# Kernel tuning notes

Measured on AMD Instinct MI355X. Metric: run time of the kernel, lower is better.

Reference implementation:

```python
import jax, jax.numpy as jnp
import numpy as np

THRESHOLD = 1.25
CURRENT_DECAY = 0.25
VOLTAGE_DECAY = 0.03
SPIKE_PROB = 0.2


def setup_inputs() -> dict:
    key = jax.random.key(0)
    k1, k2 = jax.random.split(key)
    B, N, T = 2048, 16, 1024
    # binary input spike trains [batch, neurons, time]
    spike = (jax.random.uniform(k1, (B, N, T)) < SPIKE_PROB).astype(jnp.float32)
    # Dense synapse weight [out, in], no bias (lava-dl Dense default)
    W = jax.random.normal(k2, (N, N), dtype=jnp.float32) / np.sqrt(N)
    return {"spike": spike, "W": W}


def _cuba_dense(spike, W):
    # synaptic current input per timestep: z[b,o,t]
    z = jnp.einsum('oi,bit->bot', W, spike)
    zt = jnp.moveaxis(z, -1, 0)  # [T, B, O] for scan over time

    def step(carry, x):
        c, v = carry
        c = c * (1.0 - CURRENT_DECAY) + x
        v = v * (1.0 - VOLTAGE_DECAY) + c
        s = (v >= THRESHOLD).astype(v.dtype)
        v = v * (1.0 - s)  # hard reset to zero on spike
        return (c, v), s

    zero = jnp.zeros_like(zt[0])
    _, s = jax.lax.scan(step, (zero, zero), zt)  # s: [T, B, O]
    return jnp.moveaxis(s, 0, -1)  # [B, O, T]


def reference(spike, W):
    y = _cuba_dense(spike, W)  # [B, O, T] binary spikes
    # log-cosh free energy: exp(sum_neurons log(2 cosh(y))) -> [B, T]
    return jnp.exp(jnp.sum(jnp.log(2.0 * jnp.cosh(y)), axis=1))
```

## Files before the change

kernel.cpp:

```cpp
#include <hip/hip_runtime.h>
#include <stdint.h>

#define T_STEPS 1024
#define NWORDS  256
#define NB      8
#define SCAN_BLOCK (NB * 16)

typedef float f32x4 __attribute__((ext_vector_type(4)));

__global__ __launch_bounds__(256) void k_maskify(const float* __restrict__ spike,
                                                 unsigned long long* __restrict__ masks,
                                                 const float* __restrict__ W,
                                                 double* __restrict__ tab,
                                                 int B) {
    const int b  = blockIdx.x;
    const int tc = threadIdx.x;
    if (b < B) {
        const float4* sp = reinterpret_cast<const float4*>(spike) + (size_t)b * (16 * NWORDS);
        unsigned int m0 = 0, m1 = 0, m2 = 0, m3 = 0;
#pragma unroll
        for (int i = 0; i < 16; ++i) {
            float4 v = sp[i * NWORDS + tc];
            m0 |= (v.x >= 0.5f) ? (1u << i) : 0u;
            m1 |= (v.y >= 0.5f) ? (1u << i) : 0u;
            m2 |= (v.z >= 0.5f) ? (1u << i) : 0u;
            m3 |= (v.w >= 0.5f) ? (1u << i) : 0u;
        }
        masks[(size_t)b * NWORDS + tc] =
            (unsigned long long)m0 | ((unsigned long long)m1 << 16) |
            ((unsigned long long)m2 << 32) | ((unsigned long long)m3 << 48);
    } else {
        const int o = tc & 15;
        double w[16];
#pragma unroll
        for (int j = 0; j < 16; ++j) w[j] = (double)W[o * 16 + j];
#pragma unroll
        for (int k = 0; k < 32; ++k) {
            const int e    = tc + k * 256;
            const int byte = (e >> 4) & 255;
            const int s    = k >> 4;
            double slo = 0.0, shi = 0.0;
#pragma unroll
            for (int j = 0; j < 4; ++j) slo += (byte & (1 << j))  ? w[8 * s + j]     : 0.0;
#pragma unroll
            for (int j = 0; j < 4; ++j) shi += (byte & (16 << j)) ? w[8 * s + 4 + j] : 0.0;
            tab[s * 4096 + byte * 16 + o] = slo + shi;
        }
    }
}

__global__ __launch_bounds__(SCAN_BLOCK, 1) void k_scan(const double* __restrict__ tab,
                                                        const unsigned long long* __restrict__ masks,
                                                        float* __restrict__ out) {
    const int tid = threadIdx.x;
    const int bb  = tid >> 4;
    const int o   = tid & 15;
    const int b   = blockIdx.x * NB + bb;

    const uint64_t tb     = (uint64_t)tab;
    const uint64_t mb     = (uint64_t)masks;
    const uint64_t ob_out = (uint64_t)out;
    const uint32_t ob0    = (uint32_t)(o * 8);
    const uint32_t ob1    = ob0 + 32768u;
    const uint32_t vb_m   = (uint32_t)(b * (NWORDS * 8));
    const uint32_t vb_out = (uint32_t)(b * (T_STEPS * 4));
    const int grp_sh      = tid & 48;
    const bool writer     = (o == 0);

    double c = 0.0, v = 0.0;

    double TA_0, TA_1, TA_2, TA_3, TA_4, TA_5, TA_6, TA_7;
    double TB_0, TB_1, TB_2, TB_3, TB_4, TB_5, TB_6, TB_7;
    unsigned long long MA, MB, MC, MD, q0, q1;

#define GLT(DST, VOFF) \
    asm volatile("global_load_dwordx2 %0, %1, %2" : "=v"(DST) : "v"(VOFF), "s"(tb))
#define GLM(DST, IDX) do { int _mi = (IDX); if (_mi > 255) _mi = 255;                 \
    const uint32_t _vo = vb_m + ((uint32_t)_mi << 3);                                 \
    asm volatile("global_load_dwordx2 %0, %1, %2" : "=v"(DST) : "v"(_vo), "s"(mb)); } while (0)
#define WAITV(N) asm volatile("s_waitcnt vmcnt(" #N ")" ::: "memory")
#define SBAR __builtin_amdgcn_sched_barrier(0)

#define TISSUE(P, MW) do {                                                            \
    const uint32_t _lo = (uint32_t)(MW), _hi = (uint32_t)((MW) >> 32);                \
    uint32_t _a;                                                                      \
    _a = ob0 + ((_lo & 255u) << 7);          GLT(P##_0, _a);                          \
    _a = ob1 + (((_lo >> 8) & 255u) << 7);   GLT(P##_1, _a);                          \
    _a = ob0 + (((_lo >> 16) & 255u) << 7);  GLT(P##_2, _a);                          \
    _a = ob1 + ((_lo >> 24) << 7);           GLT(P##_3, _a);                          \
    _a = ob0 + ((_hi & 255u) << 7);          GLT(P##_4, _a);                          \
    _a = ob1 + (((_hi >> 8) & 255u) << 7);   GLT(P##_5, _a);                          \
    _a = ob0 + (((_hi >> 16) & 255u) << 7);  GLT(P##_6, _a);                          \
    _a = ob1 + ((_hi >> 24) << 7);           GLT(P##_7, _a);                          \
} while (0)

#define ZSTEP(ZL, ZH, OWEL) do {                                                      \
    const double _z = (ZL) + (ZH);                                                    \
    c = fma(c, 0.75, _z);                                                             \
    v = fma(v, 0.97, c);                                                              \
    const bool _s = (v >= 1.25);                                                      \
    const unsigned long long _bal = __ballot(_s);                                     \
    v = _s ? 0.0 : v;                                                                 \
    const uint32_t _k = __popc((uint32_t)(_bal >> grp_sh) & 0xFFFFu);                 \
    OWEL = exp2f(fmaf((float)_k, 0.62581400f, 16.0f));                                \
} while (0)

#define COMPUTE(P, WD) do {                                                           \
    f32x4 _ow;                                                                        \
    ZSTEP(P##_0, P##_1, _ow.x);                                                       \
    ZSTEP(P##_2, P##_3, _ow.y);                                                       \
    ZSTEP(P##_4, P##_5, _ow.z);                                                       \
    ZSTEP(P##_6, P##_7, _ow.w);                                                       \
    if (writer) {                                                                     \
        const uint32_t _vo = vb_out + ((uint32_t)(WD) << 4);                          \
        asm volatile("global_store_dwordx4 %0, %1, %2"                                \
                     :: "v"(_vo), "v"(_ow), "s"(ob_out) : "memory");                  \
    }                                                                                 \
} while (0)

#define BODY(WD, P, MU, MI) do {                                                      \
    GLM(MI, (WD) + 4);                                                                \
    WAITV(11); SBAR;                                                                  \
    COMPUTE(P, WD);                                                                   \
    TISSUE(P, MU); SBAR;                                                              \
} while (0)

    asm volatile("s_waitcnt vmcnt(0) lgkmcnt(0)" ::: "memory");

    GLM(q0, 0); GLM(q1, 1); GLM(MA, 2); GLM(MB, 3);
    WAITV(2); SBAR;
    TISSUE(TA, q0);
    TISSUE(TB, q1); SBAR;

    GLM(MC, 4);
    WAITV(9); SBAR;
    COMPUTE(TA, 0);
    TISSUE(TA, MA); SBAR;

    GLM(MD, 5);
    WAITV(11); SBAR;
    COMPUTE(TB, 1);
    TISSUE(TB, MB); SBAR;

    for (int w = 2; w < 254; w += 4) {
        BODY(w,     TA, MC, MA);
        BODY(w + 1, TB, MD, MB);
        BODY(w + 2, TA, MA, MC);
        BODY(w + 3, TB, MB, MD);
    }

    WAITV(10); SBAR;
    COMPUTE(TA, 254);
    WAITV(1); SBAR;
    COMPUTE(TB, 255);
    asm volatile("s_waitcnt vmcnt(0)" ::: "memory");

#undef GLT
#undef GLM
#undef WAITV
#undef SBAR
#undef TISSUE
#undef ZSTEP
#undef COMPUTE
#undef BODY
}

__global__ __launch_bounds__(SCAN_BLOCK) void k_scan_fb(const float* __restrict__ W,
                                                        const float* __restrict__ spike,
                                                        float* __restrict__ out) {
    __shared__ double ztab[4][16][16];
    __shared__ unsigned long long mlds[NB][NWORDS];
    __shared__ float outtab[17];
    const int tid = threadIdx.x, bb = tid >> 4, o = tid & 15;
    for (int e = tid; e < 4 * 16 * 16; e += SCAN_BLOCK) {
        const int oo = e & 15, idx = (e >> 4) & 15, seg = e >> 8;
        double s = 0.0;
#pragma unroll
        for (int j = 0; j < 4; ++j)
            if (idx & (1 << j)) s += (double)W[oo * 16 + seg * 4 + j];
        ztab[seg][idx][oo] = s;
    }
    if (tid < 17) {
        const double ln2 = 0.69314718055994530941723212145818;
        const double l2c1 = log(2.0 * cosh(1.0));
        outtab[tid] = (float)exp((16.0 - (double)tid) * ln2 + (double)tid * l2c1);
    }
    {
        const int part = tid & 15;
        const float4* spb = reinterpret_cast<const float4*>(spike) +
                            (size_t)(blockIdx.x * NB + bb) * (16 * NWORDS);
        for (int w = 0; w < 16; ++w) {
            const int tc = part * 16 + w;
            unsigned int m0 = 0, m1 = 0, m2 = 0, m3 = 0;
#pragma unroll
            for (int i = 0; i < 16; ++i) {
                float4 v = spb[i * NWORDS + tc];
                m0 |= (v.x >= 0.5f) ? (1u << i) : 0u;
                m1 |= (v.y >= 0.5f) ? (1u << i) : 0u;
                m2 |= (v.z >= 0.5f) ? (1u << i) : 0u;
                m3 |= (v.w >= 0.5f) ? (1u << i) : 0u;
            }
            mlds[bb][tc] = (unsigned long long)m0 | ((unsigned long long)m1 << 16) |
                           ((unsigned long long)m2 << 32) | ((unsigned long long)m3 << 48);
        }
    }
    __syncthreads();
    double c = 0.0, v = 0.0;
    const int b = blockIdx.x * NB + bb;
    float* outp = out + (size_t)b * T_STEPS;
    const int grp_sh = tid & 48;
    const bool writer = (o == 0);
    for (int tg = 0; tg < NWORDS; ++tg) {
        const unsigned long long mw = mlds[bb][tg];
#pragma unroll
        for (int j = 0; j < 4; ++j) {
            const unsigned int m = (unsigned int)(mw >> (16 * j)) & 0xFFFFu;
            const double z = (ztab[0][m & 15][o] + ztab[1][(m >> 4) & 15][o]) +
                             (ztab[2][(m >> 8) & 15][o] + ztab[3][(m >> 12) & 15][o]);
            c = fma(c, 0.75, z);
            v = fma(v, 0.97, c);
            const bool s = (v >= 1.25);
            const unsigned long long bal = __ballot(s);
            v = s ? 0.0 : v;
            if (writer) outp[tg * 4 + j] = outtab[(int)__popcll((bal >> grp_sh) & 0xFFFFull)];
        }
    }
}

extern "C" void kernel_launch(void* const* d_in, const int* in_sizes, int n_in,
                              void* d_out, int out_size, void* d_ws, size_t ws_size,
                              hipStream_t stream) {
    const float* spike = (const float*)d_in[0];
    const float* W     = (const float*)d_in[1];
    float* out         = (float*)d_out;

    const int B = in_sizes[0] / (16 * T_STEPS);

    const size_t mask_bytes = (size_t)B * NWORDS * sizeof(unsigned long long);
    const size_t tab_bytes  = 2 * 256 * 16 * sizeof(double);

    if (ws_size >= mask_bytes + tab_bytes) {
        unsigned long long* masks = (unsigned long long*)d_ws;
        double* tab = (double*)((char*)d_ws + mask_bytes);
        k_maskify<<<B + 1, 256, 0, stream>>>(spike, masks, W, tab, B);
        k_scan<<<B / NB, SCAN_BLOCK, 0, stream>>>(tab, masks, out);
    } else {
        k_scan_fb<<<B / NB, SCAN_BLOCK, 0, stream>>>(W, spike, out);
    }
}
```

Measured before the change: 90.81 us.

## Interleave two independent batch recurrences per thread in scan kernel

Result: slower. 150.9 us (+66.2%).

```diff
diff --git a/kernel.cpp b/kernel.cpp
--- a/kernel.cpp
+++ b/kernel.cpp
@@ -3,8 +3,7 @@
 
 #define T_STEPS 1024
 #define NWORDS  256
-#define NB      8
-#define SCAN_BLOCK (NB * 16)
+#define SCAN_BLOCK 64
 
 typedef float f32x4 __attribute__((ext_vector_type(4)));
 
@@ -55,28 +54,33 @@
     const int tid = threadIdx.x;
     const int bb  = tid >> 4;
     const int o   = tid & 15;
-    const int b   = blockIdx.x * NB + bb;
+    const int bx  = blockIdx.x * 8 + bb;
+    const int by  = bx + 4;
 
     const uint64_t tb     = (uint64_t)tab;
     const uint64_t mb     = (uint64_t)masks;
     const uint64_t ob_out = (uint64_t)out;
     const uint32_t ob0    = (uint32_t)(o * 8);
     const uint32_t ob1    = ob0 + 32768u;
-    const uint32_t vb_m   = (uint32_t)(b * (NWORDS * 8));
-    const uint32_t vb_out = (uint32_t)(b * (T_STEPS * 4));
+    const uint32_t vb_mx  = (uint32_t)(bx * (NWORDS * 8));
+    const uint32_t vb_my  = (uint32_t)(by * (NWORDS * 8));
+    const uint32_t vb_ox  = (uint32_t)(bx * (T_STEPS * 4));
+    const uint32_t vb_oy  = (uint32_t)(by * (T_STEPS * 4));
     const int grp_sh      = tid & 48;
     const bool writer     = (o == 0);
 
-    double c = 0.0, v = 0.0;
-
-    double TA_0, TA_1, TA_2, TA_3, TA_4, TA_5, TA_6, TA_7;
-    double TB_0, TB_1, TB_2, TB_3, TB_4, TB_5, TB_6, TB_7;
-    unsigned long long MA, MB, MC, MD, q0, q1;
+    double cx = 0.0, vx = 0.0, cy = 0.0, vy = 0.0;
+
+    double TAx_0, TAx_1, TAx_2, TAx_3, TAx_4, TAx_5, TAx_6, TAx_7;
+    double TBx_0, TBx_1, TBx_2, TBx_3, TBx_4, TBx_5, TBx_6, TBx_7;
+    double TAy_0, TAy_1, TAy_2, TAy_3, TAy_4, TAy_5, TAy_6, TAy_7;
+    double TBy_0, TBy_1, TBy_2, TBy_3, TBy_4, TBy_5, TBy_6, TBy_7;
+    unsigned long long MAx, MBx, MCx, MDx, MAy, MBy, MCy, MDy, qx0, qx1, qy0, qy1;
 
 #define GLT(DST, VOFF) \
     asm volatile("global_load_dwordx2 %0, %1, %2" : "=v"(DST) : "v"(VOFF), "s"(tb))
-#define GLM(DST, IDX) do { int _mi = (IDX); if (_mi > 255) _mi = 255;                 \
-    const uint32_t _vo = vb_m + ((uint32_t)_mi << 3);                                 \
+#define GLM(DST, IDX, VBM) do { int _mi = (IDX); if (_mi > 255) _mi = 255;            \
+    const uint32_t _vo = (VBM) + ((uint32_t)_mi << 3);                                \
     asm volatile("global_load_dwordx2 %0, %1, %2" : "=v"(DST) : "v"(_vo), "s"(mb)); } while (0)
 #define WAITV(N) asm volatile("s_waitcnt vmcnt(" #N ")" ::: "memory")
 #define SBAR __builtin_amdgcn_sched_barrier(0)
@@ -94,65 +98,73 @@
     _a = ob1 + ((_hi >> 24) << 7);           GLT(P##_7, _a);                          \
 } while (0)
 
-#define ZSTEP(ZL, ZH, OWEL) do {                                                      \
+#define ZSTEP(CC, VV, ZL, ZH, OWEL) do {                                              \
     const double _z = (ZL) + (ZH);                                                    \
-    c = fma(c, 0.75, _z);                                                             \
-    v = fma(v, 0.97, c);                                                              \
-    const bool _s = (v >= 1.25);                                                      \
+    CC = fma(CC, 0.75, _z);                                                           \
+    VV = fma(VV, 0.97, CC);                                                           \
+    const bool _s = (VV >= 1.25);                                                     \
     const unsigned long long _bal = __ballot(_s);                                     \
-    v = _s ? 0.0 : v;                                                                 \
+    VV = _s ? 0.0 : VV;                                                               \
     const uint32_t _k = __popc((uint32_t)(_bal >> grp_sh) & 0xFFFFu);                 \
     OWEL = exp2f(fmaf((float)_k, 0.62581400f, 16.0f));                                \
 } while (0)
 
-#define COMPUTE(P, WD) do {                                                           \
+#define COMPUTE(P, WD, CC, VV, VBOUT) do {                                            \
     f32x4 _ow;                                                                        \
-    ZSTEP(P##_0, P##_1, _ow.x);                                                       \
-    ZSTEP(P##_2, P##_3, _ow.y);                                                       \
-    ZSTEP(P##_4, P##_5, _ow.z);                                                       \
-    ZSTEP(P##_6, P##_7, _ow.w);                                                       \
+    ZSTEP(CC, VV, P##_0, P##_1, _ow.x);                                               \
+    ZSTEP(CC, VV, P##_2, P##_3, _ow.y);                                               \
+    ZSTEP(CC, VV, P##_4, P##_5, _ow.z);                                               \
+    ZSTEP(CC, VV, P##_6, P##_7, _ow.w);                                               \
     if (writer) {                                                                     \
-        const uint32_t _vo = vb_out + ((uint32_t)(WD) << 4);                          \
+        const uint32_t _vo = (VBOUT) + ((uint32_t)(WD) << 4);                         \
         asm volatile("global_store_dwordx4 %0, %1, %2"                                \
                      :: "v"(_vo), "v"(_ow), "s"(ob_out) : "memory");                  \
     }                                                                                 \
 } while (0)
 
-#define BODY(WD, P, MU, MI) do {                                                      \
-    GLM(MI, (WD) + 4);                                                                \
-    WAITV(11); SBAR;                                                                  \
-    COMPUTE(P, WD);                                                                   \
-    TISSUE(P, MU); SBAR;                                                              \
+#define BODY(WD, P, MUX, MUY, MIX, MIY) do {                                          \
+    GLM(MIX, (WD) + 4, vb_mx);                                                        \
+    GLM(MIY, (WD) + 4, vb_my);                                                        \
+    WAITV(22); SBAR;                                                                  \
+    COMPUTE(P##x, WD, cx, vx, vb_ox);                                                 \
+    COMPUTE(P##y, WD, cy, vy, vb_oy);                                                 \
+    TISSUE(P##x, MUX);                                                                \
+    TISSUE(P##y, MUY); SBAR;                                                          \
 } while (0)
 
     asm volatile("s_waitcnt vmcnt(0) lgkmcnt(0)" ::: "memory");
 
-    GLM(q0, 0); GLM(q1, 1); GLM(MA, 2); GLM(MB, 3);
+    GLM(qx0, 0, vb_mx); GLM(qy0, 0, vb_my); GLM(qx1, 1, vb_mx); GLM(qy1, 1, vb_my);
+    GLM(MAx, 2, vb_mx); GLM(MAy, 2, vb_my); GLM(MBx, 3, vb_mx); GLM(MBy, 3, vb_my);
+    WAITV(4); SBAR;
+    TISSUE(TAx, qx0); TISSUE(TAy, qy0);
+    TISSUE(TBx, qx1); TISSUE(TBy, qy1); SBAR;
+
+    GLM(MCx, 4, vb_mx); GLM(MCy, 4, vb_my);
+    WAITV(18); SBAR;
+    COMPUTE(TAx, 0, cx, vx, vb_ox);
+    COMPUTE(TAy, 0, cy, vy, vb_oy);
+    TISSUE(TAx, MAx); TISSUE(TAy, MAy); SBAR;
+
+    GLM(MDx, 5, vb_mx); GLM(MDy, 5, vb_my);
+    WAITV(22); SBAR;
+    COMPUTE(TBx, 1, cx, vx, vb_ox);
+    COMPUTE(TBy, 1, cy, vy, vb_oy);
+    TISSUE(TBx, MBx); TISSUE(TBy, MBy); SBAR;
+
+    for (int w = 2; w < 254; w += 4) {
+        BODY(w,     TA, MCx, MCy, MAx, MAy);
+        BODY(w + 1, TB, MDx, MDy, MBx, MBy);
+        BODY(w + 2, TA, MAx, MAy, MCx, MCy);
+        BODY(w + 3, TB, MBx, MBy, MDx, MDy);
+    }
+
+    WAITV(20); SBAR;
+    COMPUTE(TAx, 254, cx, vx, vb_ox);
+    COMPUTE(TAy, 254, cy, vy, vb_oy);
     WAITV(2); SBAR;
-    TISSUE(TA, q0);
-    TISSUE(TB, q1); SBAR;
-
-    GLM(MC, 4);
-    WAITV(9); SBAR;
-    COMPUTE(TA, 0);
-    TISSUE(TA, MA); SBAR;
-
-    GLM(MD, 5);
-    WAITV(11); SBAR;
-    COMPUTE(TB, 1);
-    TISSUE(TB, MB); SBAR;
-
-    for (int w = 2; w < 254; w += 4) {
-        BODY(w,     TA, MC, MA);
-        BODY(w + 1, TB, MD, MB);
-        BODY(w + 2, TA, MA, MC);
-        BODY(w + 3, TB, MB, MD);
-    }
-
-    WAITV(10); SBAR;
-    COMPUTE(TA, 254);
-    WAITV(1); SBAR;
-    COMPUTE(TB, 255);
+    COMPUTE(TBx, 255, cx, vx, vb_ox);
+    COMPUTE(TBy, 255, cy, vy, vb_oy);
     asm volatile("s_waitcnt vmcnt(0)" ::: "memory");
 
 #undef GLT
@@ -165,14 +177,14 @@
 #undef BODY
 }
 
-__global__ __launch_bounds__(SCAN_BLOCK) void k_scan_fb(const float* __restrict__ W,
-                                                        const float* __restrict__ spike,
-                                                        float* __restrict__ out) {
+__global__ __launch_bounds__(128) void k_scan_fb(const float* __restrict__ W,
+                                                 const float* __restrict__ spike,
+                                                 float* __restrict__ out) {
     __shared__ double ztab[4][16][16];
-    __shared__ unsigned long long mlds[NB][NWORDS];
+    __shared__ unsigned long long mlds[8][NWORDS];
     __shared__ float outtab[17];
     const int tid = threadIdx.x, bb = tid >> 4, o = tid & 15;
-    for (int e = tid; e < 4 * 16 * 16; e += SCAN_BLOCK) {
+    for (int e = tid; e < 4 * 16 * 16; e += 128) {
         const int oo = e & 15, idx = (e >> 4) & 15, seg = e >> 8;
         double s = 0.0;
 #pragma unroll
@@ -188,7 +200,7 @@
     {
         const int part = tid & 15;
         const float4* spb = reinterpret_cast<const float4*>(spike) +
-                            (size_t)(blockIdx.x * NB + bb) * (16 * NWORDS);
+                            (size_t)(blockIdx.x * 8 + bb) * (16 * NWORDS);
         for (int w = 0; w < 16; ++w) {
             const int tc = part * 16 + w;
             unsigned int m0 = 0, m1 = 0, m2 = 0, m3 = 0;
@@ -206,7 +218,7 @@
     }
     __syncthreads();
     double c = 0.0, v = 0.0;
-    const int b = blockIdx.x * NB + bb;
+    const int b = blockIdx.x * 8 + bb;
     float* outp = out + (size_t)b * T_STEPS;
     const int grp_sh = tid & 48;
     const bool writer = (o == 0);
@@ -243,8 +255,8 @@
         unsigned long long* masks = (unsigned long long*)d_ws;
         double* tab = (double*)((char*)d_ws + mask_bytes);
         k_maskify<<<B + 1, 256, 0, stream>>>(spike, masks, W, tab, B);
-        k_scan<<<B / NB, SCAN_BLOCK, 0, stream>>>(tab, masks, out);
+        k_scan<<<B / 8, SCAN_BLOCK, 0, stream>>>(tab, masks, out);
     } else {
-        k_scan_fb<<<B / NB, SCAN_BLOCK, 0, stream>>>(W, spike, out);
-    }
-}
+        k_scan_fb<<<B / 8, 128, 0, stream>>>(W, spike, out);
+    }
+}
```

## Move scan lookup table and spike masks into LDS, building table per block

Applied to the files above, without the earlier changes.

After: 95.61 us. 1.05x slower.

```diff
diff --git a/kernel.cpp b/kernel.cpp
--- a/kernel.cpp
+++ b/kernel.cpp
@@ -9,60 +9,64 @@
 typedef float f32x4 __attribute__((ext_vector_type(4)));
 
 __global__ __launch_bounds__(256) void k_maskify(const float* __restrict__ spike,
-                                                 unsigned long long* __restrict__ masks,
-                                                 const float* __restrict__ W,
-                                                 double* __restrict__ tab,
-                                                 int B) {
+                                                 unsigned long long* __restrict__ masks) {
     const int b  = blockIdx.x;
     const int tc = threadIdx.x;
-    if (b < B) {
-        const float4* sp = reinterpret_cast<const float4*>(spike) + (size_t)b * (16 * NWORDS);
-        unsigned int m0 = 0, m1 = 0, m2 = 0, m3 = 0;
-#pragma unroll
-        for (int i = 0; i < 16; ++i) {
-            float4 v = sp[i * NWORDS + tc];
-            m0 |= (v.x >= 0.5f) ? (1u << i) : 0u;
-            m1 |= (v.y >= 0.5f) ? (1u << i) : 0u;
-            m2 |= (v.z >= 0.5f) ? (1u << i) : 0u;
-            m3 |= (v.w >= 0.5f) ? (1u << i) : 0u;
-        }
-        masks[(size_t)b * NWORDS + tc] =
-            (unsigned long long)m0 | ((unsigned long long)m1 << 16) |
-            ((unsigned long long)m2 << 32) | ((unsigned long long)m3 << 48);
-    } else {
-        const int o = tc & 15;
-        double w[16];
-#pragma unroll
-        for (int j = 0; j < 16; ++j) w[j] = (double)W[o * 16 + j];
-#pragma unroll
-        for (int k = 0; k < 32; ++k) {
-            const int e    = tc + k * 256;
-            const int byte = (e >> 4) & 255;
-            const int s    = k >> 4;
-            double slo = 0.0, shi = 0.0;
-#pragma unroll
-            for (int j = 0; j < 4; ++j) slo += (byte & (1 << j))  ? w[8 * s + j]     : 0.0;
-#pragma unroll
-            for (int j = 0; j < 4; ++j) shi += (byte & (16 << j)) ? w[8 * s + 4 + j] : 0.0;
-            tab[s * 4096 + byte * 16 + o] = slo + shi;
-        }
-    }
-}
-
-__global__ __launch_bounds__(SCAN_BLOCK, 1) void k_scan(const double* __restrict__ tab,
+    const float4* sp = reinterpret_cast<const float4*>(spike) + (size_t)b * (16 * NWORDS);
+    unsigned int m0 = 0, m1 = 0, m2 = 0, m3 = 0;
+#pragma unroll
+    for (int i = 0; i < 16; ++i) {
+        float4 v = sp[i * NWORDS + tc];
+        m0 |= (v.x >= 0.5f) ? (1u << i) : 0u;
+        m1 |= (v.y >= 0.5f) ? (1u << i) : 0u;
+        m2 |= (v.z >= 0.5f) ? (1u << i) : 0u;
+        m3 |= (v.w >= 0.5f) ? (1u << i) : 0u;
+    }
+    masks[(size_t)b * NWORDS + tc] =
+        (unsigned long long)m0 | ((unsigned long long)m1 << 16) |
+        ((unsigned long long)m2 << 32) | ((unsigned long long)m3 << 48);
+}
+
+__global__ __launch_bounds__(SCAN_BLOCK, 1) void k_scan(const float* __restrict__ W,
                                                         const unsigned long long* __restrict__ masks,
                                                         float* __restrict__ out) {
+    __shared__ double ztab8[2][256][17];
+    __shared__ unsigned long long mlds[NB][NWORDS + 1];
+
     const int tid = threadIdx.x;
     const int bb  = tid >> 4;
     const int o   = tid & 15;
     const int b   = blockIdx.x * NB + bb;
 
-    const uint64_t tb     = (uint64_t)tab;
-    const uint64_t mb     = (uint64_t)masks;
+    {
+        double w[16];
+#pragma unroll
+        for (int j = 0; j < 16; ++j) w[j] = (double)W[o * 16 + j];
+#pragma unroll
+        for (int k = 0; k < 64; ++k) {
+            const int e    = tid + k * SCAN_BLOCK;
+            const int byte = (e >> 4) & 255;
+            const int s    = k >> 5;
+            double slo = 0.0, shi = 0.0;
+#pragma unroll
+            for (int j = 0; j < 4; ++j) slo += (byte & (1 << j))  ? w[8 * s + j]     : 0.0;
+#pragma unroll
+            for (int j = 0; j < 4; ++j) shi += (byte & (16 << j)) ? w[8 * s + 4 + j] : 0.0;
+            ztab8[s][byte][o] = slo + shi;
+        }
+    }
+    {
+        const unsigned long long* src = masks + (size_t)blockIdx.x * NB * NWORDS;
+        for (int e = tid; e < NB * NWORDS; e += SCAN_BLOCK)
+            mlds[e >> 8][e & 255] = src[e];
+    }
+    __syncthreads();
+
+    const uint32_t tl0 = (uint32_t)(uintptr_t)(&ztab8[0][0][0]) + (uint32_t)(o * 8);
+    const uint32_t tl1 = (uint32_t)(uintptr_t)(&ztab8[1][0][0]) + (uint32_t)(o * 8);
+    const uint32_t mlb = (uint32_t)(uintptr_t)(&mlds[bb][0]);
+
     const uint64_t ob_out = (uint64_t)out;
-    const uint32_t ob0    = (uint32_t)(o * 8);
-    const uint32_t ob1    = ob0 + 32768u;
-    const uint32_t vb_m   = (uint32_t)(b * (NWORDS * 8));
     const uint32_t vb_out = (uint32_t)(b * (T_STEPS * 4));
     const int grp_sh      = tid & 48;
     const bool writer     = (o == 0);
@@ -73,25 +77,24 @@
     double TB_0, TB_1, TB_2, TB_3, TB_4, TB_5, TB_6, TB_7;
     unsigned long long MA, MB, MC, MD, q0, q1;
 
-#define GLT(DST, VOFF) \
-    asm volatile("global_load_dwordx2 %0, %1, %2" : "=v"(DST) : "v"(VOFF), "s"(tb))
-#define GLM(DST, IDX) do { int _mi = (IDX); if (_mi > 255) _mi = 255;                 \
-    const uint32_t _vo = vb_m + ((uint32_t)_mi << 3);                                 \
-    asm volatile("global_load_dwordx2 %0, %1, %2" : "=v"(DST) : "v"(_vo), "s"(mb)); } while (0)
-#define WAITV(N) asm volatile("s_waitcnt vmcnt(" #N ")" ::: "memory")
+#define DSR(DST, ADDR) asm volatile("ds_read_b64 %0, %1" : "=v"(DST) : "v"(ADDR))
+#define DSRM(DST, IDX) do { int _mi = (IDX); if (_mi > 255) _mi = 255;                \
+    const uint32_t _a = mlb + ((uint32_t)_mi << 3); DSR(DST, _a); } while (0)
+#define WAITLG(N) asm volatile("s_waitcnt lgkmcnt(" #N ")" ::: "memory")
+#define WAITV(N)  asm volatile("s_waitcnt vmcnt(" #N ")" ::: "memory")
 #define SBAR __builtin_amdgcn_sched_barrier(0)
 
 #define TISSUE(P, MW) do {                                                            \
     const uint32_t _lo = (uint32_t)(MW), _hi = (uint32_t)((MW) >> 32);                \
     uint32_t _a;                                                                      \
-    _a = ob0 + ((_lo & 255u) << 7);          GLT(P##_0, _a);                          \
-    _a = ob1 + (((_lo >> 8) & 255u) << 7);   GLT(P##_1, _a);                          \
-    _a = ob0 + (((_lo >> 16) & 255u) << 7);  GLT(P##_2, _a);                          \
-    _a = ob1 + ((_lo >> 24) << 7);           GLT(P##_3, _a);                          \
-    _a = ob0 + ((_hi & 255u) << 7);          GLT(P##_4, _a);                          \
-    _a = ob1 + (((_hi >> 8) & 255u) << 7);   GLT(P##_5, _a);                          \
-    _a = ob0 + (((_hi >> 16) & 255u) << 7);  GLT(P##_6, _a);                          \
-    _a = ob1 + ((_hi >> 24) << 7);           GLT(P##_7, _a);                          \
+    _a = tl0 + (_lo & 255u) * 136u;         DSR(P##_0, _a);                           \
+    _a = tl1 + ((_lo >> 8) & 255u) * 136u;  DSR(P##_1, _a);                           \
+    _a = tl0 + ((_lo >> 16) & 255u) * 136u; DSR(P##_2, _a);                           \
+    _a = tl1 + (_lo >> 24) * 136u;          DSR(P##_3, _a);                           \
+    _a = tl0 + (_hi & 255u) * 136u;         DSR(P##_4, _a);                           \
+    _a = tl1 + ((_hi >> 8) & 255u) * 136u;  DSR(P##_5, _a);                           \
+    _a = tl0 + ((_hi >> 16) & 255u) * 136u; DSR(P##_6, _a);                           \
+    _a = tl1 + (_hi >> 24) * 136u;          DSR(P##_7, _a);                           \
 } while (0)
 
 #define ZSTEP(ZL, ZH, OWEL) do {                                                      \
@@ -119,44 +122,37 @@
 } while (0)
 
 #define BODY(WD, P, MU, MI) do {                                                      \
-    GLM(MI, (WD) + 4);                                                                \
-    WAITV(11); SBAR;                                                                  \
+    WAITLG(9); WAITV(16); SBAR;           \
     COMPUTE(P, WD);                                                                   \
-    TISSUE(P, MU); SBAR;                                                              \
+    TISSUE(P, MU);                            \
+    DSRM(MI, (WD) + 4); SBAR;                                                         \
 } while (0)
 
     asm volatile("s_waitcnt vmcnt(0) lgkmcnt(0)" ::: "memory");
 
-    GLM(q0, 0); GLM(q1, 1); GLM(MA, 2); GLM(MB, 3);
-    WAITV(2); SBAR;
-    TISSUE(TA, q0);
-    TISSUE(TB, q1); SBAR;
-
-    GLM(MC, 4);
-    WAITV(9); SBAR;
-    COMPUTE(TA, 0);
-    TISSUE(TA, MA); SBAR;
-
-    GLM(MD, 5);
-    WAITV(11); SBAR;
-    COMPUTE(TB, 1);
-    TISSUE(TB, MB); SBAR;
-
-    for (int w = 2; w < 254; w += 4) {
-        BODY(w,     TA, MC, MA);
-        BODY(w + 1, TB, MD, MB);
-        BODY(w + 2, TA, MA, MC);
-        BODY(w + 3, TB, MB, MD);
-    }
-
-    WAITV(10); SBAR;
+    DSRM(q0, 0); DSRM(q1, 1);
+    WAITLG(0); SBAR;
+    TISSUE(TA, q0); DSRM(MA, 2);
+    TISSUE(TB, q1); DSRM(MB, 3); SBAR;
+
+    for (int w = 0; w < 252; w += 4) {
+        BODY(w,     TA, MA, MC);
+        BODY(w + 1, TB, MB, MD);
+        BODY(w + 2, TA, MC, MA);
+        BODY(w + 3, TB, MD, MB);
+    }
+    BODY(252, TA, MA, MC);
+    BODY(253, TB, MB, MD);
+
+    WAITLG(9); SBAR;
     COMPUTE(TA, 254);
-    WAITV(1); SBAR;
+    WAITLG(0); SBAR;
     COMPUTE(TB, 255);
     asm volatile("s_waitcnt vmcnt(0)" ::: "memory");
 
-#undef GLT
-#undef GLM
+#undef DSR
+#undef DSRM
+#undef WAITLG
 #undef WAITV
 #undef SBAR
 #undef TISSUE
@@ -237,13 +233,11 @@
     const int B = in_sizes[0] / (16 * T_STEPS);
 
     const size_t mask_bytes = (size_t)B * NWORDS * sizeof(unsigned long long);
-    const size_t tab_bytes  = 2 * 256 * 16 * sizeof(double);
-
-    if (ws_size >= mask_bytes + tab_bytes) {
+
+    if (ws_size >= mask_bytes) {
         unsigned long long* masks = (unsigned long long*)d_ws;
-        double* tab = (double*)((char*)d_ws + mask_bytes);
-        k_maskify<<<B + 1, 256, 0, stream>>>(spike, masks, W, tab, B);
-        k_scan<<<B / NB, SCAN_BLOCK, 0, stream>>>(tab, masks, out);
+        k_maskify<<<B, 256, 0, stream>>>(spike, masks);
+        k_scan<<<B / NB, SCAN_BLOCK, 0, stream>>>(W, masks, out);
     } else {
         k_scan_fb<<<B / NB, SCAN_BLOCK, 0, stream>>>(W, spike, out);
     }
```
